# Optimization experiments

Hardware: AMD Instinct MI355X
Metric: run time of the kernel (lower is better)

Reference implementation:

```python
import jax, jax.numpy as jnp
import numpy as np

N, D, M = 65536, 1024, 32768

def setup_inputs() -> dict:
    key = jax.random.key(0)
    k1, k2, k3, k4, k5 = jax.random.split(key, 5)
    var = jax.random.randint(k1, (N, D), -128, 128, dtype=jnp.int8)
    var_scale = jax.random.uniform(k2, (1,), jnp.float32) * 0.02 + 0.01
    indices = jax.random.randint(k3, (M, D), 0, N, dtype=jnp.int32)
    updates = (jax.random.normal(k4, (M, D)) ).astype(jnp.float16)
    smooth_scales = (jax.random.uniform(k5, (D,)) + 0.5).astype(jnp.float16)
    return {"var": var, "var_scale": var_scale, "indices": indices,
            "updates": updates, "smooth_scales": smooth_scales}

def reference(var, var_scale, indices, updates, smooth_scales):
    # dequantize int8 var with fp32 scale
    out = var.astype(jnp.float32) * var_scale  # [N, D]
    # smooth-scale the updates, promote to fp32
    upd = (updates * smooth_scales).astype(jnp.float32)  # [M, D]
    # torch scatter_add_ along axis 0: out[indices[i,j], j] += upd[i,j]
    cols = jnp.arange(out.shape[1])[None, :]  # [1, D] broadcasts vs [M, D] indices
    out = out.at[indices, cols].add(upd)
    # global abs-max -> dynamic requantization to int8
    max_val = jnp.max(jnp.abs(out))
    new_scale = max_val / 127.0
    y = jnp.clip(jnp.round(out / new_scale), -128, 127).astype(jnp.int8)
    return (y, out, new_scale[None])
```

## Files before the change

kernel.cpp:

```cpp
#include <hip/hip_runtime.h>
#include <hip/hip_fp16.h>

#define N_ROWS 65536
#define D_COLS 1024
#define M_ROWS 32768
#define QROWS  16384

using u32 = unsigned int;
using u16 = unsigned short;
typedef float f32x4 __attribute__((ext_vector_type(4)));
typedef int   i32x4 __attribute__((ext_vector_type(4)));

static __device__ __forceinline__ __half2 u32_as_half2(u32 w) {
    union { u32 u; __half2 h; } c; c.u = w; return c.h;
}

__global__ void init_ws_k(u32* ws) {
    if (threadIdx.x == 0 && blockIdx.x == 0) ws[0] = 0u;
}

__global__ __launch_bounds__(256) void t_pack_k(const int* __restrict__ idx,
                                                const float* __restrict__ upd,
                                                const float* __restrict__ scl,
                                                u32* __restrict__ packed) {
    __shared__ u32   sidx[64][65];
    __shared__ float supd[64][65];
    const int swz = (int)(blockIdx.x & 7) * 1024 + (int)(blockIdx.x >> 3);
    const int i0 = (swz & 511) * 64;
    const int j0 = (swz >> 9) * 64;
    const int t = threadIdx.x;

    {
        const int rr = t >> 2, c4 = t & 3;
        const int*   ip = idx + (size_t)(i0 + rr) * D_COLS + j0;
        const float* up = upd + (size_t)(i0 + rr) * D_COLS + j0;
        #pragma unroll
        for (int cq = 0; cq < 4; ++cq) {
            const int jc = cq * 16 + c4 * 4;
            const i32x4 iv = __builtin_nontemporal_load((const i32x4*)(ip + jc));
            const f32x4 uv = __builtin_nontemporal_load((const f32x4*)(up + jc));
            sidx[rr][jc] = (u32)iv.x; sidx[rr][jc+1] = (u32)iv.y;
            sidx[rr][jc+2] = (u32)iv.z; sidx[rr][jc+3] = (u32)iv.w;
            supd[rr][jc] = uv.x; supd[rr][jc+1] = uv.y;
            supd[rr][jc+2] = uv.z; supd[rr][jc+3] = uv.w;
        }
    }
    __syncthreads();

    {
        const int jj = t >> 2, seg = t & 3;
        const __half hs = __float2half(scl[j0 + jj]);
        u32 w16[16];
        #pragma unroll
        for (int p = 0; p < 16; ++p) {
            const int r = seg * 16 + p;
            const __half hv = __hmul(__float2half(supd[r][jj]), hs);
            w16[p] = (sidx[r][jj] & 0xffffu) | ((u32)__half_as_ushort(hv) << 16);
        }
        u32* d = packed + (size_t)(j0 + jj) * M_ROWS + i0 + seg * 16;
        ((uint4*)d)[0] = uint4{w16[0],  w16[1],  w16[2],  w16[3]};
        ((uint4*)d)[1] = uint4{w16[4],  w16[5],  w16[6],  w16[7]};
        ((uint4*)d)[2] = uint4{w16[8],  w16[9],  w16[10], w16[11]};
        ((uint4*)d)[3] = uint4{w16[12], w16[13], w16[14], w16[15]};
    }
}

__global__ __launch_bounds__(1024) void scatter_q_k(const u32* __restrict__ packed,
                                                    __half* __restrict__ sumT) {
    __shared__ float acc[QROWS];
    const int bid = (blockIdx.x & 7) * 512 + (blockIdx.x >> 3);
    const int j = bid >> 2;
    const int h = bid & 3;
    const int tid = threadIdx.x;

    float4* a4 = (float4*)acc;
    #pragma unroll
    for (int k = 0; k < 4; ++k) a4[k * 1024 + tid] = float4{0.f, 0.f, 0.f, 0.f};

    const i32x4* col4 = (const i32x4*)(packed + (size_t)j * M_ROWS);
    __syncthreads();

    #pragma unroll
    for (int k = 0; k < 8; ++k) {
        const i32x4 e4 = col4[k * 1024 + tid];
        const u32 e[4] = {(u32)e4.x, (u32)e4.y, (u32)e4.z, (u32)e4.w};
        #pragma unroll
        for (int q = 0; q < 4; ++q) {
            const int r = (int)(e[q] & 0xffffu);
            if ((r >> 14) == h)
                atomicAdd(&acc[r & (QROWS - 1)],
                          __half2float(__ushort_as_half((u16)(e[q] >> 16))));
        }
    }
    __syncthreads();

    uint4* dst4 = (uint4*)(sumT + (size_t)j * N_ROWS + h * QROWS);
    #pragma unroll
    for (int o = 0; o < 2; ++o) {
        const int base = o * 8192 + tid * 8;
        const float4 f0 = *(const float4*)&acc[base];
        const float4 f1 = *(const float4*)&acc[base + 4];
        const __half2 h0 = __floats2half2_rn(f0.x, f0.y);
        const __half2 h1 = __floats2half2_rn(f0.z, f0.w);
        const __half2 h2 = __floats2half2_rn(f1.x, f1.y);
        const __half2 h3 = __floats2half2_rn(f1.z, f1.w);
        dst4[o * 1024 + tid] = uint4{*(const u32*)&h0, *(const u32*)&h1,
                                     *(const u32*)&h2, *(const u32*)&h3};
    }
}

__global__ __launch_bounds__(256) void finalize_k(const int* __restrict__ var,
                                                  const __half* __restrict__ sumT,
                                                  const float* __restrict__ var_scale,
                                                  float* __restrict__ outf,
                                                  u32* __restrict__ ws) {
    __shared__ __half2 smh[64][68];
    __shared__ float wmax[4];
    const int swz = (int)(blockIdx.x & 7) * 1024 + (int)(blockIdx.x >> 3);
    const int r0 = (swz & 511) * 128;
    const int j0 = (swz >> 9) * 64;
    const int tid = threadIdx.x;
    const float s = var_scale[0];

    {
        const int jj = tid >> 2, seg = tid & 3;
        const __half* colp = sumT + (size_t)(j0 + jj) * N_ROWS + r0 + seg * 32;
        #pragma unroll
        for (int q = 0; q < 4; ++q) {
            const i32x4 w = __builtin_nontemporal_load((const i32x4*)colp + q);
            const u32 w0 = (u32)w.x, w1 = (u32)w.y, w2 = (u32)w.z, w3 = (u32)w.w;
            smh[seg * 16 + q * 4 + 0][jj] = u32_as_half2(w0);
            smh[seg * 16 + q * 4 + 1][jj] = u32_as_half2(w1);
            smh[seg * 16 + q * 4 + 2][jj] = u32_as_half2(w2);
            smh[seg * 16 + q * 4 + 3][jj] = u32_as_half2(w3);
        }
    }
    __syncthreads();

    float m = 0.f;
    #pragma unroll
    for (int k = 0; k < 8; ++k) {
        const int l = k * 256 + tid;
        const int rr = l >> 4, c4 = l & 15;
        const i32x4 v = __builtin_nontemporal_load(
            (const i32x4*)(var + (size_t)(r0 + rr) * D_COLS + j0) + c4);
        const __half2* hp = &smh[rr >> 1][c4 * 4];
        const __half2 p0 = hp[0], p1 = hp[1], p2 = hp[2], p3 = hp[3];
        const bool hi = (rr & 1) != 0;
        float4 o;
        o.x = (float)v.x * s + (hi ? __high2float(p0) : __low2float(p0));
        o.y = (float)v.y * s + (hi ? __high2float(p1) : __low2float(p1));
        o.z = (float)v.z * s + (hi ? __high2float(p2) : __low2float(p2));
        o.w = (float)v.w * s + (hi ? __high2float(p3) : __low2float(p3));
        ((float4*)(outf + (size_t)(r0 + rr) * D_COLS + j0))[c4] = o;
        m = fmaxf(m, fmaxf(fmaxf(fabsf(o.x), fabsf(o.y)),
                           fmaxf(fabsf(o.z), fabsf(o.w))));
    }
    for (int off = 32; off; off >>= 1) m = fmaxf(m, __shfl_xor(m, off));
    if ((tid & 63) == 0) wmax[tid >> 6] = m;
    __syncthreads();
    if (tid == 0) {
        m = fmaxf(fmaxf(wmax[0], wmax[1]), fmaxf(wmax[2], wmax[3]));
        atomicMax(ws, __float_as_uint(m));
    }
}

__global__ __launch_bounds__(256) void quant_k(const float* __restrict__ outf,
                                               float* __restrict__ y,
                                               const u32* __restrict__ ws,
                                               float* __restrict__ scale_out) {
    const float mx = __uint_as_float(ws[0]);
    const float inv = 127.0f / mx;
    const int i_rev = 1023 - (int)(blockIdx.x >> 3);
    const int swz = (int)(blockIdx.x & 7) * 1024 + i_rev;
    const int r0 = (swz & 511) * 128;
    const int j0 = (swz >> 9) * 64;
    const int tid = threadIdx.x;
    if (blockIdx.x == 0 && tid == 0) scale_out[0] = mx / 127.0f;
    #pragma unroll
    for (int k = 0; k < 8; ++k) {
        const int l = k * 256 + tid;
        const int rr = l >> 4, c4 = l & 15;
        const size_t off = (size_t)(r0 + rr) * D_COLS + j0 + c4 * 4;
        const float4 v = *(const float4*)(outf + off);
        f32x4 o;
        o.x = fminf(fmaxf(rintf(v.x * inv), -128.f), 127.f);
        o.y = fminf(fmaxf(rintf(v.y * inv), -128.f), 127.f);
        o.z = fminf(fmaxf(rintf(v.z * inv), -128.f), 127.f);
        o.w = fminf(fmaxf(rintf(v.w * inv), -128.f), 127.f);
        __builtin_nontemporal_store(o, (f32x4*)(y + off));
    }
}

extern "C" void kernel_launch(void* const* d_in, const int* in_sizes, int n_in,
                              void* d_out, int out_size, void* d_ws, size_t ws_size,
                              hipStream_t stream) {
    const int*   var       = (const int*)d_in[0];
    const float* var_scale = (const float*)d_in[1];
    const int*   idx       = (const int*)d_in[2];
    const float* upd       = (const float*)d_in[3];
    const float* scl       = (const float*)d_in[4];

    float* y    = (float*)d_out;
    float* outf = y + (size_t)N_ROWS * D_COLS;
    float* scale_out = y + 2 * (size_t)N_ROWS * D_COLS;

    u32*    packed = (u32*)y;
    __half* sumT   = (__half*)((char*)y + (size_t)134217728);
    u32* ws = (u32*)d_ws;

    init_ws_k<<<1, 64, 0, stream>>>(ws);
    t_pack_k<<<8192, 256, 0, stream>>>(idx, upd, scl, packed);
    scatter_q_k<<<4096, 1024, 0, stream>>>(packed, sumT);
    finalize_k<<<8192, 256, 0, stream>>>(var, sumT, var_scale, outf, ws);
    quant_k<<<8192, 256, 0, stream>>>(outf, y, ws, scale_out);
}
```

Measured before the change: 486.0 us.

## Persist finalize blocks over four row tiles with double-buffered LDS prefetch

finalize_k now launches a quarter as many blocks, and each block walks four consecutive 128-row tiles. The next tile's transposed fp16 sums are prefetched into registers while the current tile is processed, then written into the other half of a double-buffered shared array. This is meant to hide the sumT load latency and cut per-block launch overhead, at the cost of more LDS, extra syncs and less parallelism. The quant_k block order also drops its reversed traversal, which changes L2 reuse of the outf data left by finalize.

```diff
diff --git a/kernel.cpp b/kernel.cpp
--- a/kernel.cpp
+++ b/kernel.cpp
@@ -5,6 +5,7 @@
 #define D_COLS 1024
 #define M_ROWS 32768
 #define QROWS  16384
+#define FT     4
 
 using u32 = unsigned int;
 using u16 = unsigned short;
@@ -114,47 +115,75 @@
                                                   const float* __restrict__ var_scale,
                                                   float* __restrict__ outf,
                                                   u32* __restrict__ ws) {
-    __shared__ __half2 smh[64][68];
+    __shared__ __half2 smh[2][64][68];
     __shared__ float wmax[4];
-    const int swz = (int)(blockIdx.x & 7) * 1024 + (int)(blockIdx.x >> 3);
-    const int r0 = (swz & 511) * 128;
-    const int j0 = (swz >> 9) * 64;
+    const int swz = (int)(blockIdx.x & 7) * 256 + (int)(blockIdx.x >> 3);
+    const int ub = (swz & 127) * (FT * 128);
+    const int j0 = (swz >> 7) * 64;
     const int tid = threadIdx.x;
     const float s = var_scale[0];
-
+    const int jj = tid >> 2, seg = tid & 3;
+
+    i32x4 rg[4];
     {
-        const int jj = tid >> 2, seg = tid & 3;
-        const __half* colp = sumT + (size_t)(j0 + jj) * N_ROWS + r0 + seg * 32;
+        const __half* colp = sumT + (size_t)(j0 + jj) * N_ROWS + ub + seg * 32;
+        #pragma unroll
+        for (int q = 0; q < 4; ++q)
+            rg[q] = __builtin_nontemporal_load((const i32x4*)colp + q);
         #pragma unroll
         for (int q = 0; q < 4; ++q) {
-            const i32x4 w = __builtin_nontemporal_load((const i32x4*)colp + q);
-            const u32 w0 = (u32)w.x, w1 = (u32)w.y, w2 = (u32)w.z, w3 = (u32)w.w;
-            smh[seg * 16 + q * 4 + 0][jj] = u32_as_half2(w0);
-            smh[seg * 16 + q * 4 + 1][jj] = u32_as_half2(w1);
-            smh[seg * 16 + q * 4 + 2][jj] = u32_as_half2(w2);
-            smh[seg * 16 + q * 4 + 3][jj] = u32_as_half2(w3);
+            const u32 w0 = (u32)rg[q].x, w1 = (u32)rg[q].y;
+            const u32 w2 = (u32)rg[q].z, w3 = (u32)rg[q].w;
+            smh[0][seg * 16 + q * 4 + 0][jj] = u32_as_half2(w0);
+            smh[0][seg * 16 + q * 4 + 1][jj] = u32_as_half2(w1);
+            smh[0][seg * 16 + q * 4 + 2][jj] = u32_as_half2(w2);
+            smh[0][seg * 16 + q * 4 + 3][jj] = u32_as_half2(w3);
         }
     }
     __syncthreads();
 
     float m = 0.f;
     #pragma unroll
-    for (int k = 0; k < 8; ++k) {
-        const int l = k * 256 + tid;
-        const int rr = l >> 4, c4 = l & 15;
-        const i32x4 v = __builtin_nontemporal_load(
-            (const i32x4*)(var + (size_t)(r0 + rr) * D_COLS + j0) + c4);
-        const __half2* hp = &smh[rr >> 1][c4 * 4];
-        const __half2 p0 = hp[0], p1 = hp[1], p2 = hp[2], p3 = hp[3];
-        const bool hi = (rr & 1) != 0;
-        float4 o;
-        o.x = (float)v.x * s + (hi ? __high2float(p0) : __low2float(p0));
-        o.y = (float)v.y * s + (hi ? __high2float(p1) : __low2float(p1));
-        o.z = (float)v.z * s + (hi ? __high2float(p2) : __low2float(p2));
-        o.w = (float)v.w * s + (hi ? __high2float(p3) : __low2float(p3));
-        ((float4*)(outf + (size_t)(r0 + rr) * D_COLS + j0))[c4] = o;
-        m = fmaxf(m, fmaxf(fmaxf(fabsf(o.x), fabsf(o.y)),
-                           fmaxf(fabsf(o.z), fabsf(o.w))));
+    for (int t = 0; t < FT; ++t) {
+        const int cur = t & 1;
+        const int r0 = ub + t * 128;
+        if (t + 1 < FT) {
+            const __half* colp = sumT + (size_t)(j0 + jj) * N_ROWS + (r0 + 128) + seg * 32;
+            #pragma unroll
+            for (int q = 0; q < 4; ++q)
+                rg[q] = __builtin_nontemporal_load((const i32x4*)colp + q);
+        }
+        #pragma unroll
+        for (int k = 0; k < 8; ++k) {
+            const int l = k * 256 + tid;
+            const int rr = l >> 4, c4 = l & 15;
+            const i32x4 v = __builtin_nontemporal_load(
+                (const i32x4*)(var + (size_t)(r0 + rr) * D_COLS + j0) + c4);
+            const __half2* hp = &smh[cur][rr >> 1][c4 * 4];
+            const __half2 p0 = hp[0], p1 = hp[1], p2 = hp[2], p3 = hp[3];
+            const bool hi = (rr & 1) != 0;
+            float4 o;
+            o.x = (float)v.x * s + (hi ? __high2float(p0) : __low2float(p0));
+            o.y = (float)v.y * s + (hi ? __high2float(p1) : __low2float(p1));
+            o.z = (float)v.z * s + (hi ? __high2float(p2) : __low2float(p2));
+            o.w = (float)v.w * s + (hi ? __high2float(p3) : __low2float(p3));
+            ((float4*)(outf + (size_t)(r0 + rr) * D_COLS + j0))[c4] = o;
+            m = fmaxf(m, fmaxf(fmaxf(fabsf(o.x), fabsf(o.y)),
+                               fmaxf(fabsf(o.z), fabsf(o.w))));
+        }
+        __syncthreads();
+        if (t + 1 < FT) {
+            #pragma unroll
+            for (int q = 0; q < 4; ++q) {
+                const u32 w0 = (u32)rg[q].x, w1 = (u32)rg[q].y;
+                const u32 w2 = (u32)rg[q].z, w3 = (u32)rg[q].w;
+                smh[cur ^ 1][seg * 16 + q * 4 + 0][jj] = u32_as_half2(w0);
+                smh[cur ^ 1][seg * 16 + q * 4 + 1][jj] = u32_as_half2(w1);
+                smh[cur ^ 1][seg * 16 + q * 4 + 2][jj] = u32_as_half2(w2);
+                smh[cur ^ 1][seg * 16 + q * 4 + 3][jj] = u32_as_half2(w3);
+            }
+            __syncthreads();
+        }
     }
     for (int off = 32; off; off >>= 1) m = fmaxf(m, __shfl_xor(m, off));
     if ((tid & 63) == 0) wmax[tid >> 6] = m;
@@ -171,8 +200,7 @@
                                                float* __restrict__ scale_out) {
     const float mx = __uint_as_float(ws[0]);
     const float inv = 127.0f / mx;
-    const int i_rev = 1023 - (int)(blockIdx.x >> 3);
-    const int swz = (int)(blockIdx.x & 7) * 1024 + i_rev;
+    const int swz = (int)(blockIdx.x & 7) * 1024 + (int)(blockIdx.x >> 3);
     const int r0 = (swz & 511) * 128;
     const int j0 = (swz >> 9) * 64;
     const int tid = threadIdx.x;
@@ -212,6 +240,6 @@
     init_ws_k<<<1, 64, 0, stream>>>(ws);
     t_pack_k<<<8192, 256, 0, stream>>>(idx, upd, scl, packed);
     scatter_q_k<<<4096, 1024, 0, stream>>>(packed, sumT);
-    finalize_k<<<8192, 256, 0, stream>>>(var, sumT, var_scale, outf, ws);
+    finalize_k<<<2048, 256, 0, stream>>>(var, sumT, var_scale, outf, ws);
     quant_k<<<8192, 256, 0, stream>>>(outf, y, ws, scale_out);
 }
```

After: 479.3 us, median of 2. About the same (-1.4%).
